# Performance work log

Measured on AMD Instinct MI355X. Metric: run time of the kernel, lower is better.

Reference implementation:

```python
import jax, jax.numpy as jnp
import numpy as np

WH, WW, WD = 4, 4, 4
NUM_HEADS = 12


def _relative_coords():
    # (3, N) flattened coords of the 3D window, N = WH*WW*WD
    g = jnp.stack(jnp.meshgrid(jnp.arange(WH), jnp.arange(WW), jnp.arange(WD), indexing='ij'), axis=0)
    flat = g.reshape(3, -1)
    rel = flat[:, :, None] - flat[:, None, :]          # (3, N, N)
    return jnp.transpose(rel, (1, 2, 0)).astype(jnp.float32)  # (N, N, 3)


def setup_inputs() -> dict:
    key = jax.random.key(0)
    ks = jax.random.split(key, 9)
    B_, N, C = 2048, WH * WW * WD, 384
    s = lambda fan: 1.0 / np.sqrt(fan)
    return {
        'x': jax.random.normal(ks[0], (B_, N, C), jnp.float32),
        'qkv_w': jax.random.normal(ks[1], (C, 3 * C), jnp.float32) * s(C),
        'qkv_b': jax.random.normal(ks[2], (3 * C,), jnp.float32) * 0.02,
        'proj_w': jax.random.normal(ks[3], (C, C), jnp.float32) * s(C),
        'proj_b': jax.random.normal(ks[4], (C,), jnp.float32) * 0.02,
        'mlp_w1': jax.random.normal(ks[5], (3, 64), jnp.float32) * s(3),
        'mlp_b1': jax.random.normal(ks[6], (64,), jnp.float32) * 0.02,
        'mlp_w2': jax.random.normal(ks[7], (64, NUM_HEADS), jnp.float32) * s(64),
        'mlp_b2': jax.random.normal(ks[8], (NUM_HEADS,), jnp.float32) * 0.02,
    }


def reference(x, qkv_w, qkv_b, proj_w, proj_b, mlp_w1, mlp_b1, mlp_w2, mlp_b2):
    B_, N, C = x.shape
    H = NUM_HEADS
    hd = C // H
    scale = hd ** -0.5

    qkv = (x @ qkv_w + qkv_b).reshape(B_, N, 3, H, hd)
    q, k, v = qkv[:, :, 0], qkv[:, :, 1], qkv[:, :, 2]   # (B_, N, H, hd)

    # MLP-based relative position bias: (N, N, 3) -> (H, N, N)
    rel = _relative_coords()
    bias = jax.nn.relu(rel @ mlp_w1 + mlp_b1) @ mlp_w2 + mlp_b2  # (N, N, H)
    bias = jnp.transpose(bias, (2, 0, 1))                        # (H, N, N)

    attn = jnp.einsum('bnhd,bmhd->bhnm', q, k) * scale + bias[None]
    attn = jax.nn.softmax(attn, axis=-1)

    out = jnp.einsum('bhnm,bmhd->bnhd', attn, v).reshape(B_, N, C)
    return out @ proj_w + proj_b
```

## Files before the change

kernel.cpp:

```cpp
#include <hip/hip_runtime.h>
#include <stdint.h>

#define SCALE 0.17677669529663687f

typedef __attribute__((ext_vector_type(8))) short short8;
typedef __attribute__((ext_vector_type(4))) float floatx4;

__device__ __forceinline__ unsigned short f2bf(float f) {
    union { float f; unsigned u; } v; v.f = f;
    unsigned r = (v.u + 0x7fffu + ((v.u >> 16) & 1u)) >> 16;
    return (unsigned short)r;
}

__global__ void prep_weights(const float* __restrict__ qkv_w,
                             const float* __restrict__ proj_w,
                             unsigned short* __restrict__ qkv_wt,
                             unsigned short* __restrict__ proj_wt) {
    int i = blockIdx.x * blockDim.x + threadIdx.x;
    const int nq = 1152 * 384;
    const int np = 384 * 384;
    if (i < nq) {
        int r = i / 384, c = i - r * 384;
        qkv_wt[i] = f2bf(qkv_w[c * 1152 + r]);
    } else if (i < nq + np) {
        int o = i - nq;
        int r = o / 384, c = o - r * 384;
        proj_wt[o] = f2bf(proj_w[c * 384 + r]);
    }
}

__global__ void prep_bias(const float* __restrict__ w1, const float* __restrict__ b1,
                          const float* __restrict__ w2, const float* __restrict__ b2,
                          float* __restrict__ bt) {
    int t = blockIdx.x * blockDim.x + threadIdx.x;
    int i = t >> 6, j = t & 63;
    float r0 = (float)((i >> 4) - (j >> 4));
    float r1 = (float)(((i >> 2) & 3) - ((j >> 2) & 3));
    float r2 = (float)((i & 3) - (j & 3));
    float acc[12];
#pragma unroll
    for (int h = 0; h < 12; ++h) acc[h] = b2[h];
    for (int u = 0; u < 64; ++u) {
        float hv = r0 * w1[u] + r1 * w1[64 + u] + r2 * w1[128 + u] + b1[u];
        hv = fmaxf(hv, 0.f);
#pragma unroll
        for (int h = 0; h < 12; ++h) acc[h] += hv * w2[u * 12 + h];
    }
    for (int h = 0; h < 12; ++h) bt[(h << 12) + (i << 6) + j] = acc[h];
}

#define XP  392
#define QKP 40
#define VTP 72
#define PBP 72
#define OSP 72

__launch_bounds__(384, 2)
__global__ void win_attn(const float* __restrict__ x,
                         const unsigned short* __restrict__ qkv_wt,
                         const float* __restrict__ qkv_b,
                         const unsigned short* __restrict__ proj_wt,
                         const float* __restrict__ proj_b,
                         const float* __restrict__ bt,
                         float* __restrict__ out) {
    __shared__ unsigned short xs[64 * XP];
    __shared__ unsigned short ql[2][2][64 * QKP];
    __shared__ unsigned short kl[2][2][64 * QKP];
    __shared__ unsigned short vt[2][2][32 * VTP];
    __shared__ unsigned short pb[2][4][16 * PBP];
    __shared__ unsigned short osl[2][64 * OSP];
    const int tid  = threadIdx.x;
    const int lane = tid & 63;
    const int w    = tid >> 6;
    const int l15  = lane & 15;
    const int quad = lane >> 4;
    const int b    = blockIdx.x;

    const float* xb = x + (size_t)b * (64 * 384);
#pragma unroll
    for (int it = 0; it < 16; ++it) {
        int idx = it * 384 + tid;
        int row = idx / 96;
        int c4  = idx - row * 96;
        const float4 v = *reinterpret_cast<const float4*>(xb + row * 384 + c4 * 4);
        uint2 pk;
        pk.x = (unsigned)f2bf(v.x) | ((unsigned)f2bf(v.y) << 16);
        pk.y = (unsigned)f2bf(v.z) | ((unsigned)f2bf(v.w) << 16);
        *reinterpret_cast<uint2*>(&xs[row * XP + c4 * 4]) = pk;
    }
    __syncthreads();

    const int j3 = w >> 1;
    const int d2 = w & 1;
    const int ntile = (w < 4) ? 5 : 2;
    const int t0    = (w < 4) ? 5 * w : (20 + 2 * (w - 4));
    const int h0  = (w < 4) ? 0 : 1;
    const int rb0 = (w < 4) ? w : (w - 4);

    const floatx4 zf4 = {0.f, 0.f, 0.f, 0.f};
    floatx4 acc2[5][4];
#pragma unroll
    for (int jj = 0; jj < 5; ++jj)
#pragma unroll
        for (int m = 0; m < 4; ++m) acc2[jj][m] = zf4;

#define PROJ_STEP(PP)                                                                   \
    {                                                                                   \
        const int buf_ = (PP) & 1;                                                      \
        short8 a2_[4][2];                                                               \
        _Pragma("unroll")                                                               \
        for (int m = 0; m < 4; ++m)                                                     \
            _Pragma("unroll")                                                           \
            for (int k2 = 0; k2 < 2; ++k2)                                              \
                a2_[m][k2] = *reinterpret_cast<const short8*>(                          \
                    &osl[buf_][(16 * m + l15) * OSP + k2 * 32 + quad * 8]);             \
        _Pragma("unroll")                                                               \
        for (int jj = 0; jj < 5; ++jj)                                                  \
            if (jj < ntile) {                                                           \
                const unsigned short* pw =                                              \
                    proj_wt + (size_t)((t0 + jj) * 16 + l15) * 384 + (PP) * 64;         \
                const short8 b20 = *reinterpret_cast<const short8*>(pw + quad * 8);     \
                const short8 b21 = *reinterpret_cast<const short8*>(pw + 32 + quad * 8);\
                _Pragma("unroll")                                                       \
                for (int m = 0; m < 4; ++m) {                                           \
                    acc2[jj][m] = __builtin_amdgcn_mfma_f32_16x16x32_bf16(              \
                        a2_[m][0], b20, acc2[jj][m], 0, 0, 0);                          \
                    acc2[jj][m] = __builtin_amdgcn_mfma_f32_16x16x32_bf16(              \
                        a2_[m][1], b21, acc2[jj][m], 0, 0, 0);                          \
                }                                                                       \
            }                                                                           \
    }

#define B23_TASK(H, RB, PP, RBUF)                                                       \
    {                                                                                   \
        const int hg_ = 2 * (PP) + (H);                                                 \
        const short8 aq_ = *reinterpret_cast<const short8*>(                            \
            &ql[RBUF][H][(16 * (RB) + l15) * QKP + quad * 8]);                          \
        floatx4 s4_[4];                                                                 \
        _Pragma("unroll")                                                               \
        for (int c = 0; c < 4; ++c) {                                                   \
            const short8 bk_ = *reinterpret_cast<const short8*>(                        \
                &kl[RBUF][H][(16 * c + l15) * QKP + quad * 8]);                         \
            s4_[c] = __builtin_amdgcn_mfma_f32_16x16x32_bf16(aq_, bk_, zf4, 0, 0, 0);   \
        }                                                                               \
        const float* bth_ = bt + ((size_t)hg_ << 12);                                   \
        float rs_[4];                                                                   \
        _Pragma("unroll")                                                               \
        for (int r = 0; r < 4; ++r) {                                                   \
            const int n_ = 16 * (RB) + quad * 4 + r;                                    \
            _Pragma("unroll")                                                           \
            for (int c = 0; c < 4; ++c)                                                 \
                s4_[c][r] = s4_[c][r] * SCALE + bth_[(n_ << 6) + 16 * c + l15];         \
            float m0_ = fmaxf(fmaxf(s4_[0][r], s4_[1][r]), fmaxf(s4_[2][r], s4_[3][r]));\
            _Pragma("unroll")                                                           \
            for (int sh = 1; sh < 16; sh <<= 1) m0_ = fmaxf(m0_, __shfl_xor(m0_, sh, 16)); \
            float p0_ = 0.f;                                                            \
            _Pragma("unroll")                                                           \
            for (int c = 0; c < 4; ++c) {                                               \
                float pv_ = __expf(s4_[c][r] - m0_);                                    \
                s4_[c][r] = pv_;                                                        \
                p0_ += pv_;                                                             \
            }                                                                           \
            _Pragma("unroll")                                                           \
            for (int sh = 1; sh < 16; sh <<= 1) p0_ += __shfl_xor(p0_, sh, 16);         \
            rs_[r] = 1.f / p0_;                                                         \
            _Pragma("unroll")                                                           \
            for (int c = 0; c < 4; ++c)                                                 \
                pb[H][RB][(quad * 4 + r) * PBP + 16 * c + l15] = f2bf(s4_[c][r]);       \
        }                                                                               \
        short8 ap_[2];                                                                  \
        _Pragma("unroll")                                                               \
        for (int kkp = 0; kkp < 2; ++kkp)                                               \
            ap_[kkp] = *reinterpret_cast<const short8*>(                                \
                &pb[H][RB][l15 * PBP + kkp * 32 + quad * 8]);                           \
        _Pragma("unroll")                                                               \
        for (int t = 0; t < 2; ++t) {                                                   \
            floatx4 oacc_ = zf4;                                                        \
            _Pragma("unroll")                                                           \
            for (int kkp = 0; kkp < 2; ++kkp) {                                         \
                const short8 bv_ = *reinterpret_cast<const short8*>(                    \
                    &vt[RBUF][H][(16 * t + l15) * VTP + kkp * 32 + quad * 8]);          \
                oacc_ = __builtin_amdgcn_mfma_f32_16x16x32_bf16(ap_[kkp], bv_, oacc_, 0, 0, 0); \
            }                                                                           \
            _Pragma("unroll")                                                           \
            for (int r = 0; r < 4; ++r)                                                 \
                osl[(PP) & 1][(16 * (RB) + quad * 4 + r) * OSP + (H) * 32 + 16 * t + l15] = \
                    f2bf(oacc_[r] * rs_[r]);                                            \
        }                                                                               \
    }

#pragma unroll 1
    for (int p = 0; p < 6; ++p) {
        const int ob = p & 1;
        {
            floatx4 acc[2][4];
#pragma unroll
            for (int hh = 0; hh < 2; ++hh)
#pragma unroll
                for (int m = 0; m < 4; ++m) acc[hh][m] = zf4;

            int colbase[2];
#pragma unroll
            for (int hh = 0; hh < 2; ++hh)
                colbase[hh] = j3 * 384 + (2 * p + hh) * 32 + d2 * 16;
            const unsigned short* wcol0 = qkv_wt + (size_t)(colbase[0] + l15) * 384;
            const unsigned short* wcol1 = qkv_wt + (size_t)(colbase[1] + l15) * 384;

#pragma unroll
            for (int kk = 0; kk < 12; ++kk) {
                short8 a[4];
#pragma unroll
                for (int m = 0; m < 4; ++m)
                    a[m] = *reinterpret_cast<const short8*>(
                        &xs[(16 * m + l15) * XP + kk * 32 + quad * 8]);
                const short8 bf0 = *reinterpret_cast<const short8*>(wcol0 + kk * 32 + quad * 8);
                const short8 bf1 = *reinterpret_cast<const short8*>(wcol1 + kk * 32 + quad * 8);
#pragma unroll
                for (int m = 0; m < 4; ++m) {
                    acc[0][m] = __builtin_amdgcn_mfma_f32_16x16x32_bf16(a[m], bf0, acc[0][m], 0, 0, 0);
                    acc[1][m] = __builtin_amdgcn_mfma_f32_16x16x32_bf16(a[m], bf1, acc[1][m], 0, 0, 0);
                }
            }
#pragma unroll
            for (int hh = 0; hh < 2; ++hh) {
                const float bc = qkv_b[colbase[hh] + l15];
                if (j3 < 2) {
                    unsigned short* dst = (j3 == 0) ? ql[ob][hh] : kl[ob][hh];
#pragma unroll
                    for (int m = 0; m < 4; ++m)
#pragma unroll
                        for (int r = 0; r < 4; ++r)
                            dst[(16 * m + quad * 4 + r) * QKP + d2 * 16 + l15] =
                                f2bf(acc[hh][m][r] + bc);
                } else {
#pragma unroll
                    for (int m = 0; m < 4; ++m) {
                        uint2 pk;
                        pk.x = (unsigned)f2bf(acc[hh][m][0] + bc) | ((unsigned)f2bf(acc[hh][m][1] + bc) << 16);
                        pk.y = (unsigned)f2bf(acc[hh][m][2] + bc) | ((unsigned)f2bf(acc[hh][m][3] + bc) << 16);
                        *reinterpret_cast<uint2*>(
                            &vt[ob][hh][(d2 * 16 + l15) * VTP + 16 * m + quad * 4]) = pk;
                    }
                }
            }
        }
        if (p >= 1) {
            const int rob = ob ^ 1;
            B23_TASK(h0, rb0, (p - 1), rob);
            if (w >= 4) B23_TASK(1, (w - 2), (p - 1), rob);
        }
        if (p >= 2) PROJ_STEP(p - 2);
        __syncthreads();
    }

    {
        B23_TASK(h0, rb0, 5, 1);
        if (w >= 4) B23_TASK(1, (w - 2), 5, 1);
        PROJ_STEP(4);
        __syncthreads();
        PROJ_STEP(5);
    }

    float* ob_ptr = out + (size_t)b * (64 * 384);
#pragma unroll
    for (int jj = 0; jj < 5; ++jj)
        if (jj < ntile) {
            const int col = (t0 + jj) * 16 + l15;
            const float pbias = proj_b[col];
#pragma unroll
            for (int m = 0; m < 4; ++m)
#pragma unroll
                for (int r = 0; r < 4; ++r)
                    ob_ptr[(16 * m + quad * 4 + r) * 384 + col] = acc2[jj][m][r] + pbias;
        }
#undef PROJ_STEP
#undef B23_TASK
}

extern "C" void kernel_launch(void* const* d_in, const int* in_sizes, int n_in,
                              void* d_out, int out_size, void* d_ws, size_t ws_size,
                              hipStream_t stream) {
    const float* x      = (const float*)d_in[0];
    const float* qkv_w  = (const float*)d_in[1];
    const float* qkv_b  = (const float*)d_in[2];
    const float* proj_w = (const float*)d_in[3];
    const float* proj_b = (const float*)d_in[4];
    const float* mlp_w1 = (const float*)d_in[5];
    const float* mlp_b1 = (const float*)d_in[6];
    const float* mlp_w2 = (const float*)d_in[7];
    const float* mlp_b2 = (const float*)d_in[8];
    float* out = (float*)d_out;

    unsigned short* qkv_wt  = (unsigned short*)d_ws;
    unsigned short* proj_wt = qkv_wt + 1152 * 384;
    float*          bt      = (float*)(proj_wt + 384 * 384);

    prep_weights<<<2304, 256, 0, stream>>>(qkv_w, proj_w, qkv_wt, proj_wt);
    prep_bias<<<16, 256, 0, stream>>>(mlp_w1, mlp_b1, mlp_w2, mlp_b2, bt);
    win_attn<<<2048, 384, 0, stream>>>(x, qkv_wt, qkv_b, proj_wt, proj_b, bt, out);
}
```

Before: 793.3 us.

## Keep softmax probabilities in registers via transposed QK^T and bpermute

The attention score tile is now computed transposed (K as A operand, Q as B), so each lane holds one query row's scores. Row max and sum then need only two cross-quad shuffles, and the bias is read with float4 loads. Probabilities are packed to bf16 with the hardware v_cvt_pk_bf16_f32 instruction and rearranged into the PV MFMA operand with ds_bpermute, which removes the shared-memory P round trip and its LDS buffer. The weight prep kernel also becomes a tiled shared-memory transpose with coalesced accesses, and other bf16 packing sites use the hardware convert. The risks are the extra bpermute traffic and a subtle operand-layout mapping that must be correct for the results to match.

Measured after the change: 739.5 us. 6.8% less time.

```diff
diff --git a/kernel.cpp b/kernel.cpp
--- a/kernel.cpp
+++ b/kernel.cpp
@@ -5,27 +5,54 @@
 
 typedef __attribute__((ext_vector_type(8))) short short8;
 typedef __attribute__((ext_vector_type(4))) float floatx4;
+typedef __attribute__((ext_vector_type(4))) unsigned uintx4;
 
 __device__ __forceinline__ unsigned short f2bf(float f) {
     union { float f; unsigned u; } v; v.f = f;
     unsigned r = (v.u + 0x7fffu + ((v.u >> 16) & 1u)) >> 16;
     return (unsigned short)r;
 }
+__device__ __forceinline__ unsigned cvtpk(float lo, float hi) {
+    unsigned d;
+    asm("v_cvt_pk_bf16_f32 %0, %1, %2" : "=v"(d) : "v"(lo), "v"(hi));
+    return d;
+}
 
 __global__ void prep_weights(const float* __restrict__ qkv_w,
                              const float* __restrict__ proj_w,
                              unsigned short* __restrict__ qkv_wt,
                              unsigned short* __restrict__ proj_wt) {
-    int i = blockIdx.x * blockDim.x + threadIdx.x;
-    const int nq = 1152 * 384;
-    const int np = 384 * 384;
-    if (i < nq) {
-        int r = i / 384, c = i - r * 384;
-        qkv_wt[i] = f2bf(qkv_w[c * 1152 + r]);
-    } else if (i < nq + np) {
-        int o = i - nq;
-        int r = o / 384, c = o - r * 384;
-        proj_wt[o] = f2bf(proj_w[c * 384 + r]);
+    __shared__ float t[32][33];
+    const int tile = blockIdx.x;
+    const int idx = threadIdx.x;
+    const int j = idx & 31, i0 = idx >> 5;
+    if (tile < 432) {
+        const int tc = tile / 36, tr = tile - tc * 36;
+#pragma unroll
+        for (int pass = 0; pass < 4; ++pass) {
+            int i = i0 + pass * 8;
+            t[i][j] = qkv_w[(tc * 32 + i) * 1152 + tr * 32 + j];
+        }
+        __syncthreads();
+#pragma unroll
+        for (int pass = 0; pass < 4; ++pass) {
+            int i = i0 + pass * 8;
+            qkv_wt[(tr * 32 + i) * 384 + tc * 32 + j] = f2bf(t[j][i]);
+        }
+    } else {
+        const int t2 = tile - 432;
+        const int tc = t2 / 12, tr = t2 - tc * 12;
+#pragma unroll
+        for (int pass = 0; pass < 4; ++pass) {
+            int i = i0 + pass * 8;
+            t[i][j] = proj_w[(tc * 32 + i) * 384 + tr * 32 + j];
+        }
+        __syncthreads();
+#pragma unroll
+        for (int pass = 0; pass < 4; ++pass) {
+            int i = i0 + pass * 8;
+            proj_wt[(tr * 32 + i) * 384 + tc * 32 + j] = f2bf(t[j][i]);
+        }
     }
 }
 
@@ -52,7 +79,6 @@
 #define XP  392
 #define QKP 40
 #define VTP 72
-#define PBP 72
 #define OSP 72
 
 __launch_bounds__(384, 2)
@@ -67,7 +93,6 @@
     __shared__ unsigned short ql[2][2][64 * QKP];
     __shared__ unsigned short kl[2][2][64 * QKP];
     __shared__ unsigned short vt[2][2][32 * VTP];
-    __shared__ unsigned short pb[2][4][16 * PBP];
     __shared__ unsigned short osl[2][64 * OSP];
     const int tid  = threadIdx.x;
     const int lane = tid & 63;
@@ -84,8 +109,8 @@
         int c4  = idx - row * 96;
         const float4 v = *reinterpret_cast<const float4*>(xb + row * 384 + c4 * 4);
         uint2 pk;
-        pk.x = (unsigned)f2bf(v.x) | ((unsigned)f2bf(v.y) << 16);
-        pk.y = (unsigned)f2bf(v.z) | ((unsigned)f2bf(v.w) << 16);
+        pk.x = cvtpk(v.x, v.y);
+        pk.y = cvtpk(v.z, v.w);
         *reinterpret_cast<uint2*>(&xs[row * XP + c4 * 4]) = pk;
     }
     __syncthreads();
@@ -133,59 +158,86 @@
 
 #define B23_TASK(H, RB, PP, RBUF)                                                       \
     {                                                                                   \
-        const int hg_ = 2 * (PP) + (H);                                                 \
-        const short8 aq_ = *reinterpret_cast<const short8*>(                            \
-            &ql[RBUF][H][(16 * (RB) + l15) * QKP + quad * 8]);                          \
-        floatx4 s4_[4];                                                                 \
+        const int n_ = 16 * (RB) + l15;                                                 \
+        const short8 bq_ = *reinterpret_cast<const short8*>(                            \
+            &ql[RBUF][H][n_ * QKP + quad * 8]);                                         \
+        floatx4 st_[4];                                                                 \
         _Pragma("unroll")                                                               \
         for (int c = 0; c < 4; ++c) {                                                   \
-            const short8 bk_ = *reinterpret_cast<const short8*>(                        \
+            const short8 ak_ = *reinterpret_cast<const short8*>(                        \
                 &kl[RBUF][H][(16 * c + l15) * QKP + quad * 8]);                         \
-            s4_[c] = __builtin_amdgcn_mfma_f32_16x16x32_bf16(aq_, bk_, zf4, 0, 0, 0);   \
-        }                                                                               \
-        const float* bth_ = bt + ((size_t)hg_ << 12);                                   \
-        float rs_[4];                                                                   \
-        _Pragma("unroll")                                                               \
-        for (int r = 0; r < 4; ++r) {                                                   \
-            const int n_ = 16 * (RB) + quad * 4 + r;                                    \
+            st_[c] = __builtin_amdgcn_mfma_f32_16x16x32_bf16(ak_, bq_, zf4, 0, 0, 0);   \
+        }                                                                               \
+        const float* bth_ = bt + ((size_t)(2 * (PP) + (H)) << 12) + (n_ << 6);          \
+        _Pragma("unroll")                                                               \
+        for (int c = 0; c < 4; ++c) {                                                   \
+            const float4 bb_ = *reinterpret_cast<const float4*>(bth_ + 16 * c + 4 * quad); \
+            st_[c][0] = st_[c][0] * SCALE + bb_.x;                                      \
+            st_[c][1] = st_[c][1] * SCALE + bb_.y;                                      \
+            st_[c][2] = st_[c][2] * SCALE + bb_.z;                                      \
+            st_[c][3] = st_[c][3] * SCALE + bb_.w;                                      \
+        }                                                                               \
+        float m0_ = st_[0][0];                                                          \
+        _Pragma("unroll")                                                               \
+        for (int c = 0; c < 4; ++c)                                                     \
             _Pragma("unroll")                                                           \
-            for (int c = 0; c < 4; ++c)                                                 \
-                s4_[c][r] = s4_[c][r] * SCALE + bth_[(n_ << 6) + 16 * c + l15];         \
-            float m0_ = fmaxf(fmaxf(s4_[0][r], s4_[1][r]), fmaxf(s4_[2][r], s4_[3][r]));\
+            for (int r = 0; r < 4; ++r) m0_ = fmaxf(m0_, st_[c][r]);                    \
+        m0_ = fmaxf(m0_, __shfl_xor(m0_, 16));                                          \
+        m0_ = fmaxf(m0_, __shfl_xor(m0_, 32));                                          \
+        float p0_ = 0.f;                                                                \
+        float p_[4][4];                                                                 \
+        _Pragma("unroll")                                                               \
+        for (int c = 0; c < 4; ++c)                                                     \
             _Pragma("unroll")                                                           \
-            for (int sh = 1; sh < 16; sh <<= 1) m0_ = fmaxf(m0_, __shfl_xor(m0_, sh, 16)); \
-            float p0_ = 0.f;                                                            \
-            _Pragma("unroll")                                                           \
-            for (int c = 0; c < 4; ++c) {                                               \
-                float pv_ = __expf(s4_[c][r] - m0_);                                    \
-                s4_[c][r] = pv_;                                                        \
-                p0_ += pv_;                                                             \
+            for (int r = 0; r < 4; ++r) {                                               \
+                p_[c][r] = __expf(st_[c][r] - m0_);                                     \
+                p0_ += p_[c][r];                                                        \
             }                                                                           \
-            _Pragma("unroll")                                                           \
-            for (int sh = 1; sh < 16; sh <<= 1) p0_ += __shfl_xor(p0_, sh, 16);         \
-            rs_[r] = 1.f / p0_;                                                         \
-            _Pragma("unroll")                                                           \
-            for (int c = 0; c < 4; ++c)                                                 \
-                pb[H][RB][(quad * 4 + r) * PBP + 16 * c + l15] = f2bf(s4_[c][r]);       \
-        }                                                                               \
-        short8 ap_[2];                                                                  \
-        _Pragma("unroll")                                                               \
-        for (int kkp = 0; kkp < 2; ++kkp)                                               \
-            ap_[kkp] = *reinterpret_cast<const short8*>(                                \
-                &pb[H][RB][l15 * PBP + kkp * 32 + quad * 8]);                           \
+        p0_ += __shfl_xor(p0_, 16);                                                     \
+        p0_ += __shfl_xor(p0_, 32);                                                     \
+        const float rs_ = 1.f / p0_;                                                    \
+        unsigned upk_[4][2];                                                            \
+        _Pragma("unroll")                                                               \
+        for (int c = 0; c < 4; ++c) {                                                   \
+            upk_[c][0] = cvtpk(p_[c][0], p_[c][1]);                                     \
+            upk_[c][1] = cvtpk(p_[c][2], p_[c][3]);                                     \
+        }                                                                               \
+        const int addrA_ = (l15 + ((quad & 1) << 5)) << 2;                              \
+        const int addrB_ = addrA_ + 64;                                                 \
+        const bool hi_ = (quad & 2) != 0;                                               \
+        short8 bp_[2];                                                                  \
+        _Pragma("unroll")                                                               \
+        for (int kkp = 0; kkp < 2; ++kkp) {                                             \
+            const int c0_ = 2 * kkp, c1_ = c0_ + 1;                                     \
+            unsigned w0a = __builtin_amdgcn_ds_bpermute(addrA_, upk_[c0_][0]);          \
+            unsigned w0b = __builtin_amdgcn_ds_bpermute(addrA_, upk_[c1_][0]);          \
+            unsigned w1a = __builtin_amdgcn_ds_bpermute(addrA_, upk_[c0_][1]);          \
+            unsigned w1b = __builtin_amdgcn_ds_bpermute(addrA_, upk_[c1_][1]);          \
+            unsigned w2a = __builtin_amdgcn_ds_bpermute(addrB_, upk_[c0_][0]);          \
+            unsigned w2b = __builtin_amdgcn_ds_bpermute(addrB_, upk_[c1_][0]);          \
+            unsigned w3a = __builtin_amdgcn_ds_bpermute(addrB_, upk_[c0_][1]);          \
+            unsigned w3b = __builtin_amdgcn_ds_bpermute(addrB_, upk_[c1_][1]);          \
+            uintx4 uu_;                                                                 \
+            uu_.x = hi_ ? w0b : w0a;                                                    \
+            uu_.y = hi_ ? w1b : w1a;                                                    \
+            uu_.z = hi_ ? w2b : w2a;                                                    \
+            uu_.w = hi_ ? w3b : w3a;                                                    \
+            bp_[kkp] = __builtin_bit_cast(short8, uu_);                                 \
+        }                                                                               \
         _Pragma("unroll")                                                               \
         for (int t = 0; t < 2; ++t) {                                                   \
             floatx4 oacc_ = zf4;                                                        \
             _Pragma("unroll")                                                           \
             for (int kkp = 0; kkp < 2; ++kkp) {                                         \
-                const short8 bv_ = *reinterpret_cast<const short8*>(                    \
+                const short8 av_ = *reinterpret_cast<const short8*>(                    \
                     &vt[RBUF][H][(16 * t + l15) * VTP + kkp * 32 + quad * 8]);          \
-                oacc_ = __builtin_amdgcn_mfma_f32_16x16x32_bf16(ap_[kkp], bv_, oacc_, 0, 0, 0); \
+                oacc_ = __builtin_amdgcn_mfma_f32_16x16x32_bf16(av_, bp_[kkp], oacc_, 0, 0, 0); \
             }                                                                           \
-            _Pragma("unroll")                                                           \
-            for (int r = 0; r < 4; ++r)                                                 \
-                osl[(PP) & 1][(16 * (RB) + quad * 4 + r) * OSP + (H) * 32 + 16 * t + l15] = \
-                    f2bf(oacc_[r] * rs_[r]);                                            \
+            uint2 pk_;                                                                  \
+            pk_.x = cvtpk(oacc_[0] * rs_, oacc_[1] * rs_);                              \
+            pk_.y = cvtpk(oacc_[2] * rs_, oacc_[3] * rs_);                              \
+            *reinterpret_cast<uint2*>(                                                  \
+                &osl[(PP) & 1][n_ * OSP + (H) * 32 + 16 * t + 4 * quad]) = pk_;         \
         }                                                                               \
     }
 
@@ -236,8 +288,8 @@
 #pragma unroll
                     for (int m = 0; m < 4; ++m) {
                         uint2 pk;
-                        pk.x = (unsigned)f2bf(acc[hh][m][0] + bc) | ((unsigned)f2bf(acc[hh][m][1] + bc) << 16);
-                        pk.y = (unsigned)f2bf(acc[hh][m][2] + bc) | ((unsigned)f2bf(acc[hh][m][3] + bc) << 16);
+                        pk.x = cvtpk(acc[hh][m][0] + bc, acc[hh][m][1] + bc);
+                        pk.y = cvtpk(acc[hh][m][2] + bc, acc[hh][m][3] + bc);
                         *reinterpret_cast<uint2*>(
                             &vt[ob][hh][(d2 * 16 + l15) * VTP + 16 * m + quad * 4]) = pk;
                     }
@@ -295,7 +347,7 @@
     unsigned short* proj_wt = qkv_wt + 1152 * 384;
     float*          bt      = (float*)(proj_wt + 384 * 384);
 
-    prep_weights<<<2304, 256, 0, stream>>>(qkv_w, proj_w, qkv_wt, proj_wt);
+    prep_weights<<<576, 256, 0, stream>>>(qkv_w, proj_w, qkv_wt, proj_wt);
     prep_bias<<<16, 256, 0, stream>>>(mlp_w1, mlp_b1, mlp_w2, mlp_b2, bt);
     win_attn<<<2048, 384, 0, stream>>>(x, qkv_wt, qkv_b, proj_wt, proj_b, bt, out);
 }
```
